# Optimization experiments

Hardware: AMD Instinct MI355X
Metric: run time of the kernel (lower is better)

## Reference

```python
import jax, jax.numpy as jnp
import numpy as np

N_NODES = 100000
N_EDGES = 1250000
NFEAT = 64
EDGE_DIM = 13
HID = 64
NREPEATS = 3
EPS = 1e-5


def setup_inputs() -> dict:
    key = jax.random.key(0)
    ks = jax.random.split(key, 16)
    s = lambda fan_in: 1.0 / np.sqrt(fan_in)
    return {
        "hx": jax.random.normal(ks[0], (N_NODES, NFEAT), dtype=jnp.float32),
        "edge_index": jax.random.randint(ks[1], (2, N_EDGES), 0, N_NODES, dtype=jnp.int64),
        "edgefeats": jax.random.normal(ks[2], (N_EDGES, EDGE_DIM), dtype=jnp.float32),
        # fnet MLP: 13 -> 64 -> 64 -> NFEAT (last layer with bias, llbias=True)
        "fW1": jax.random.uniform(ks[3], (64, EDGE_DIM), jnp.float32, -s(EDGE_DIM), s(EDGE_DIM)),
        "fb1": jax.random.uniform(ks[4], (64,), jnp.float32, -s(EDGE_DIM), s(EDGE_DIM)),
        "fW2": jax.random.uniform(ks[5], (64, 64), jnp.float32, -s(64), s(64)),
        "fb2": jax.random.uniform(ks[6], (64,), jnp.float32, -s(64), s(64)),
        "fW3": jax.random.uniform(ks[7], (NFEAT, 64), jnp.float32, -s(64), s(64)),
        "fb3": jax.random.uniform(ks[8], (NFEAT,), jnp.float32, -s(64), s(64)),
        # GRUCellEx params
        "Wih": jax.random.uniform(ks[9], (3 * HID, NFEAT), jnp.float32, -s(HID), s(HID)),
        "Whh": jax.random.uniform(ks[10], (3 * HID, HID), jnp.float32, -s(HID), s(HID)),
        "bih": jax.random.uniform(ks[11], (3 * HID,), jnp.float32, -s(HID), s(HID)),
        "bhh": jax.random.uniform(ks[12], (3 * HID,), jnp.float32, -s(HID), s(HID)),
        "Wig": jax.random.uniform(ks[13], (NFEAT, HID), jnp.float32, -s(HID), s(HID)),
        "big": jax.random.uniform(ks[14], (NFEAT,), jnp.float32, -s(HID), s(HID)),
    }


def _inorm(g):
    # InstanceNorm1d(1 channel): normalize each row over its 3H features, biased var
    mu = jnp.mean(g, axis=-1, keepdims=True)
    var = jnp.mean(jnp.square(g - mu), axis=-1, keepdims=True)
    return (g - mu) * jax.lax.rsqrt(var + EPS)


def reference(hx, edge_index, edgefeats, fW1, fb1, fW2, fb2, fW3, fb3,
              Wih, Whh, bih, bhh, Wig, big):
    # fnet: per-edge weight vector [E, NFEAT] (vv=True)
    w = jax.nn.relu(edgefeats @ fW1.T + fb1)
    w = jax.nn.relu(w @ fW2.T + fb2)
    w = w @ fW3.T + fb3

    # flow='target_to_source': gather from edge_index[1], aggregate at edge_index[0]
    dst = edge_index[0]
    src = edge_index[1]
    deg = jax.ops.segment_sum(jnp.ones((src.shape[0],), jnp.float32), dst,
                              num_segments=hx.shape[0])
    inv_deg = 1.0 / jnp.maximum(deg, 1.0)

    bih_r, bih_i, bih_n = jnp.split(bih, 3)
    bhh_r, bhh_i, bhh_n = jnp.split(bhh, 3)

    hxs = [hx]
    for _ in range(NREPEATS):
        # NNConv (vv): message = x_j * w, mean aggregation
        msg = hx[src] * w                                   # [E, F]
        agg = jax.ops.segment_sum(msg, dst, num_segments=hx.shape[0]) * inv_deg[:, None]
        # GRUCellEx: input gate on hidden
        inp = jax.nn.sigmoid(hx @ Wig.T + big) * agg
        gi = _inorm(inp @ Wih.T)                            # [N, 3H]
        gh = _inorm(hx @ Whh.T)
        i_r, i_i, i_n = jnp.split(gi, 3, axis=1)
        h_r, h_i, h_n = jnp.split(gh, 3, axis=1)
        resetgate = jax.nn.sigmoid(i_r + bih_r + h_r + bhh_r)
        inputgate = jax.nn.sigmoid(i_i + bih_i + h_i + bhh_i)
        newgate = jnp.tanh(i_n + bih_n + resetgate * (h_n + bhh_n))
        hx = newgate + inputgate * (hx - newgate)
        hxs.append(hx)
    return jnp.concatenate(hxs, axis=1)                     # [N, F*(NREPEATS+1)]
```

## Files before the change

### kernel.cpp

```cpp
#include <hip/hip_runtime.h>
#include <math.h>

#define NN 100000
#define NE 1250000
#define EPSI 1e-5f

#define WS_W        0ull
#define WS_AGG      160000000ull
#define WS_WB       185600000ull
#define WS_INVDEG   264000000ull
#define WS_COUNTS   264400000ull
#define WS_ROWSTART 264800000ull
#define WS_CURSOR   265200128ull
#define WS_BSUM     265600128ull
#define WS_BSUMEX   265601792ull
#define WS_SRC      265603584ull
#define WS_EPERM    270603584ull

#define WB_TOTAL 37888

typedef unsigned short u16;
typedef unsigned int u32;
typedef short s16x4 __attribute__((ext_vector_type(4)));
typedef short s16x8 __attribute__((ext_vector_type(8)));
typedef float f32x4 __attribute__((ext_vector_type(4)));
typedef u32 u32x4 __attribute__((ext_vector_type(4)));
typedef u32 u32x2 __attribute__((ext_vector_type(2)));
typedef float f32x4u __attribute__((ext_vector_type(4), aligned(4)));

__device__ __forceinline__ u16 f2bf(float f) {
    u32 u = __float_as_uint(f);
    return (u16)((u + 0x7fffu + ((u >> 16) & 1u)) >> 16);
}
__device__ __forceinline__ float bf2f(u16 b) {
    return __uint_as_float(((u32)b) << 16);
}
__device__ __forceinline__ u32 cvtpk(float lo, float hi) {
    u32 r;
    asm("v_cvt_pk_bf16_f32 %0, %1, %2" : "=v"(r) : "v"(lo), "v"(hi));
    return r;
}
__device__ __forceinline__ float sigmoidf_(float x) {
    return 1.f / (1.f + __expf(-x));
}
__device__ __forceinline__ float tanhf_(float x) {
    float e = __expf(2.f * x);
    return 1.f - 2.f / (e + 1.f);
}
__device__ __forceinline__ s16x8 lds_frag(const u16* p) {
    s16x4 lo = *(const s16x4*)p;
    s16x4 hi = *(const s16x4*)(p + 4);
    return __builtin_shufflevector(lo, hi, 0, 1, 2, 3, 4, 5, 6, 7);
}
__device__ __forceinline__ s16x8 gfrag(const u16* W, int n, int ks, int q) {
    return *(const s16x8*)(W + n * 64 + ks * 32 + q * 8);
}
__device__ __forceinline__ float unpk(const u32* p, int r) {
    u32 v = p[r >> 1];
    return bf2f((u16)((r & 1) ? (v >> 16) : (v & 0xffffu)));
}

__global__ __launch_bounds__(256) void k_fnet_mfma(
    const float* __restrict__ ef,
    const float* __restrict__ b1, const float* __restrict__ b2,
    const float* __restrict__ b3,
    const int* __restrict__ eperm,
    const u16* __restrict__ wbf,
    u16* __restrict__ wout)
{
    __shared__ u16 w1l[64 * 16];
    __shared__ u16 w2l[64 * 68];
    __shared__ u16 w3l[64 * 68];
    __shared__ u16 hbuf[4][32 * 68];

    int tid = threadIdx.x;
    const u16* wf1 = wbf + 28672;
    const u16* wf2 = wbf + 29696;
    const u16* wf3 = wbf + 33792;
    if (tid < 128)
        *(u32x4*)(&w1l[tid * 8]) = *(const u32x4*)(wf1 + tid * 8);
    for (int c = tid; c < 512; c += 256) {
        int n = c >> 3, cc = c & 7;
        u32x4 v2 = *(const u32x4*)(wf2 + c * 8);
        u32x4 v3 = *(const u32x4*)(wf3 + c * 8);
        u16* p2 = &w2l[n * 68 + cc * 8];
        u16* p3 = &w3l[n * 68 + cc * 8];
        *(u32x2*)p2       = __builtin_shufflevector(v2, v2, 0, 1);
        *(u32x2*)(p2 + 4) = __builtin_shufflevector(v2, v2, 2, 3);
        *(u32x2*)p3       = __builtin_shufflevector(v3, v3, 0, 1);
        *(u32x2*)(p3 + 4) = __builtin_shufflevector(v3, v3, 2, 3);
    }
    __syncthreads();

    int wave = tid >> 6, lane = tid & 63;
    int q = lane >> 4, t = lane & 15;
    int ebase = blockIdx.x * 128 + wave * 32;
    u16* hb = hbuf[wave];

    f32x4 b1v = *(const f32x4*)(b1 + 4 * t);
    f32x4 b2v = *(const f32x4*)(b2 + 4 * t);
    f32x4 b3v = *(const f32x4*)(b3 + 4 * t);

    const s16x8 zfrag = {0, 0, 0, 0, 0, 0, 0, 0};

    s16x8 a1[2];
#pragma unroll
    for (int mi = 0; mi < 2; ++mi) {
        int e = ebase + mi * 16 + t;
        u32 xp[4] = {0u, 0u, 0u, 0u};
        if (e < NE) {
            const float* ep = ef + (size_t)e * 13;
            if (q == 0) {
                f32x4u v0 = *(const f32x4u*)(ep);
                f32x4u v1 = *(const f32x4u*)(ep + 4);
                xp[0] = cvtpk(v0[0], v0[1]); xp[1] = cvtpk(v0[2], v0[3]);
                xp[2] = cvtpk(v1[0], v1[1]); xp[3] = cvtpk(v1[2], v1[3]);
            } else if (q == 1) {
                f32x4u v0 = *(const f32x4u*)(ep + 8);
                float v12 = ep[12];
                xp[0] = cvtpk(v0[0], v0[1]); xp[1] = cvtpk(v0[2], v0[3]);
                xp[2] = cvtpk(v12, 0.f);
            }
        }
        a1[mi] = __builtin_bit_cast(s16x8, *(u32x4*)xp);
    }

    s16x8 B1f[4];
#pragma unroll
    for (int ni = 0; ni < 4; ++ni) {
        s16x8 b = zfrag;
        if (q < 2) b = lds_frag(&w1l[(ni * 16 + t) * 16 + q * 8]);
        B1f[ni] = b;
    }

    f32x4 h1[4][2];
#pragma unroll
    for (int ni = 0; ni < 4; ++ni)
#pragma unroll
        for (int mi = 0; mi < 2; ++mi) {
            f32x4 acc = {b1v[ni], b1v[ni], b1v[ni], b1v[ni]};
            acc = __builtin_amdgcn_mfma_f32_16x16x32_bf16(a1[mi], B1f[ni], acc, 0, 0, 0);
            h1[ni][mi] = acc;
        }
#pragma unroll
    for (int mi = 0; mi < 2; ++mi)
#pragma unroll
        for (int r = 0; r < 4; ++r) {
            u32 lo = cvtpk(fmaxf(h1[0][mi][r], 0.f), fmaxf(h1[1][mi][r], 0.f));
            u32 hi = cvtpk(fmaxf(h1[2][mi][r], 0.f), fmaxf(h1[3][mi][r], 0.f));
            u32x2 v = {lo, hi};
            *(u32x2*)(&hb[(mi * 16 + q * 4 + r) * 68 + 4 * t]) = v;
        }

    s16x8 a2[2][2];
#pragma unroll
    for (int mi = 0; mi < 2; ++mi)
#pragma unroll
        for (int ks = 0; ks < 2; ++ks)
            a2[mi][ks] = lds_frag(&hb[(mi * 16 + t) * 68 + ks * 32 + q * 8]);
    f32x4 h2[4][2];
#pragma unroll
    for (int ni = 0; ni < 4; ++ni) {
        s16x8 w0 = lds_frag(&w2l[(ni * 16 + t) * 68 + q * 8]);
        s16x8 w1_ = lds_frag(&w2l[(ni * 16 + t) * 68 + 32 + q * 8]);
#pragma unroll
        for (int mi = 0; mi < 2; ++mi) {
            f32x4 acc = {b2v[ni], b2v[ni], b2v[ni], b2v[ni]};
            acc = __builtin_amdgcn_mfma_f32_16x16x32_bf16(a2[mi][0], w0, acc, 0, 0, 0);
            acc = __builtin_amdgcn_mfma_f32_16x16x32_bf16(a2[mi][1], w1_, acc, 0, 0, 0);
            h2[ni][mi] = acc;
        }
    }
#pragma unroll
    for (int mi = 0; mi < 2; ++mi)
#pragma unroll
        for (int r = 0; r < 4; ++r) {
            u32 lo = cvtpk(fmaxf(h2[0][mi][r], 0.f), fmaxf(h2[1][mi][r], 0.f));
            u32 hi = cvtpk(fmaxf(h2[2][mi][r], 0.f), fmaxf(h2[3][mi][r], 0.f));
            u32x2 v = {lo, hi};
            *(u32x2*)(&hb[(mi * 16 + q * 4 + r) * 68 + 4 * t]) = v;
        }

    s16x8 a3[2][2];
#pragma unroll
    for (int mi = 0; mi < 2; ++mi)
#pragma unroll
        for (int ks = 0; ks < 2; ++ks)
            a3[mi][ks] = lds_frag(&hb[(mi * 16 + t) * 68 + ks * 32 + q * 8]);
    f32x4 h3[4][2];
#pragma unroll
    for (int ni = 0; ni < 4; ++ni) {
        s16x8 w0 = lds_frag(&w3l[(ni * 16 + t) * 68 + q * 8]);
        s16x8 w1_ = lds_frag(&w3l[(ni * 16 + t) * 68 + 32 + q * 8]);
#pragma unroll
        for (int mi = 0; mi < 2; ++mi) {
            f32x4 acc = {b3v[ni], b3v[ni], b3v[ni], b3v[ni]};
            acc = __builtin_amdgcn_mfma_f32_16x16x32_bf16(a3[mi][0], w0, acc, 0, 0, 0);
            acc = __builtin_amdgcn_mfma_f32_16x16x32_bf16(a3[mi][1], w1_, acc, 0, 0, 0);
            h3[ni][mi] = acc;
        }
    }
    int base0 = ebase + q * 4;
    int base1 = ebase + 16 + q * 4;
    int4 pos0 = *(const int4*)(eperm + ((base0 + 3 < NE) ? base0 : 0));
    int4 pos1 = *(const int4*)(eperm + ((base1 + 3 < NE) ? base1 : 0));
#pragma unroll
    for (int mi = 0; mi < 2; ++mi)
#pragma unroll
        for (int r = 0; r < 4; ++r) {
            int e = ebase + mi * 16 + q * 4 + r;
            if (e < NE) {
                int pos = mi ? ((const int*)&pos1)[r] : ((const int*)&pos0)[r];
                u32x2 v = {cvtpk(h3[0][mi][r], h3[1][mi][r]),
                           cvtpk(h3[2][mi][r], h3[3][mi][r])};
                *(u32x2*)(wout + (size_t)pos * 64 + 4 * t) = v;
            }
        }
}

__global__ void k_prep_w(const float* __restrict__ Wig, const float* __restrict__ Whh,
                         const float* __restrict__ Wih,
                         const float* __restrict__ W1, const float* __restrict__ W2,
                         const float* __restrict__ W3, u16* __restrict__ wb)
{
    int i = blockIdx.x * 256 + threadIdx.x;
    if (i >= WB_TOTAL) return;
    float v;
    if (i < 4096) {
        int n = i >> 6, k = i & 63;
        int pn = ((n & 15) << 2) + (n >> 4);
        v = Wig[pn * 64 + k];
    } else if (i < 16384) {
        int j = i - 4096;
        int n = j >> 6, k = j & 63;
        int g = n >> 6, m = n & 63;
        int pm = ((m & 15) << 2) + (m >> 4);
        v = Whh[(g * 64 + pm) * 64 + k];
    } else if (i < 28672) {
        int j = i - 16384;
        int n = j >> 6, k = j & 63;
        int g = n >> 6, m = n & 63;
        int pm = ((m & 15) << 2) + (m >> 4);
        v = Wih[(g * 64 + pm) * 64 + k];
    } else if (i < 29696) {
        int j = i - 28672;
        int n = j >> 4, k = j & 15;
        int pn = ((n & 15) << 2) + (n >> 4);
        v = (k < 13) ? W1[pn * 13 + k] : 0.f;
    } else if (i < 33792) {
        int j = i - 29696;
        int n = j >> 6, k = j & 63;
        int pn = ((n & 15) << 2) + (n >> 4);
        v = W2[pn * 64 + k];
    } else {
        int j = i - 33792;
        int n = j >> 6, k = j & 63;
        int pn = ((n & 15) << 2) + (n >> 4);
        v = W3[pn * 64 + k];
    }
    wb[i] = f2bf(v);
}

__global__ void k_count(const int* __restrict__ idx, int* __restrict__ counts)
{
    int e = blockIdx.x * 256 + threadIdx.x;
    if (e < NE) atomicAdd(&counts[idx[e]], 1);
}

__global__ void k_scan_partial(const int* __restrict__ counts, int* __restrict__ bsum)
{
    __shared__ int s[256];
    int i = blockIdx.x * 256 + threadIdx.x;
    int v = (i < NN) ? counts[i] : 0;
    s[threadIdx.x] = v; __syncthreads();
    for (int off = 128; off > 0; off >>= 1) {
        if (threadIdx.x < off) s[threadIdx.x] += s[threadIdx.x + off];
        __syncthreads();
    }
    if (threadIdx.x == 0) bsum[blockIdx.x] = s[0];
}

__global__ void k_scan_bsum(const int* __restrict__ bsum, int* __restrict__ bsumex)
{
    __shared__ int s[512];
    int t = threadIdx.x;
    int v0 = (t < 391) ? bsum[t] : 0;
    s[t] = v0; __syncthreads();
    for (int off = 1; off < 512; off <<= 1) {
        int add = (t >= off) ? s[t - off] : 0;
        __syncthreads();
        s[t] += add;
        __syncthreads();
    }
    if (t < 391) bsumex[t] = s[t] - v0;
}

__global__ void k_scan_final(const int* __restrict__ counts, const int* __restrict__ bsumex,
                             int* __restrict__ rowstart, int* __restrict__ cursor,
                             float* __restrict__ invdeg)
{
    __shared__ int s[256];
    int t = threadIdx.x;
    int i = blockIdx.x * 256 + t;
    int c = (i < NN) ? counts[i] : 0;
    s[t] = c; __syncthreads();
    for (int off = 1; off < 256; off <<= 1) {
        int add = (t >= off) ? s[t - off] : 0;
        __syncthreads();
        s[t] += add;
        __syncthreads();
    }
    int ex = s[t] - c + bsumex[blockIdx.x];
    if (i < NN) {
        rowstart[i] = ex;
        cursor[i] = ex;
        invdeg[i] = 1.f / (float)(c > 1 ? c : 1);
    }
    if (i == 0) rowstart[NN] = NE;
}

__global__ void k_scatter(const int* __restrict__ idx, int* __restrict__ cursor,
                          int* __restrict__ srcs, int* __restrict__ eperm)
{
    int e = blockIdx.x * 256 + threadIdx.x;
    if (e < NE) {
        int d = idx[e];
        int s = idx[NE + e];
        int p = atomicAdd(&cursor[d], 1);
        __builtin_nontemporal_store(s, &srcs[p]);
        eperm[e] = p;
    }
}

__global__ void k_init(const float4* __restrict__ hx4, float* __restrict__ outp)
{
    int i = blockIdx.x * 256 + threadIdx.x;
    int n = i >> 4, q = i & 15;
    ((float4*)(outp + (size_t)n * 256))[q] = hx4[i];
}

__global__ __launch_bounds__(256) void k_agg(
    const float* __restrict__ outp, const u16* __restrict__ w,
    const int* __restrict__ srcs, const int* __restrict__ rowstart,
    const float* __restrict__ invdeg, float* __restrict__ agg, int it)
{
    int lane = threadIdx.x & 63;
    int g = lane >> 4, t = lane & 15;
    int n = blockIdx.x * 4 + (threadIdx.x >> 6);
    n = __builtin_amdgcn_readfirstlane(n);
    int p0 = rowstart[n], p1 = rowstart[n + 1];
    const float* hxb = outp + (size_t)it * 64 + 4 * t;
    f32x4 accA = {0.f, 0.f, 0.f, 0.f};
    f32x4 accB = {0.f, 0.f, 0.f, 0.f};
    int p = p0;
    for (; p + 8 <= p1; p += 8) {
        int sA = srcs[p + g];
        int sB = srcs[p + 4 + g];
        f32x4 hA = *(const f32x4*)(hxb + (size_t)sA * 256);
        f32x4 hB = *(const f32x4*)(hxb + (size_t)sB * 256);
        s16x4 wA = __builtin_nontemporal_load((const s16x4*)(w + (size_t)(p + g) * 64 + 4 * t));
        s16x4 wB = __builtin_nontemporal_load((const s16x4*)(w + (size_t)(p + 4 + g) * 64 + 4 * t));
#pragma unroll
        for (int j = 0; j < 4; ++j) {
            accA[j] = fmaf(hA[j], bf2f((u16)wA[j]), accA[j]);
            accB[j] = fmaf(hB[j], bf2f((u16)wB[j]), accB[j]);
        }
    }
    if (p + 4 <= p1) {
        int sA = srcs[p + g];
        f32x4 hA = *(const f32x4*)(hxb + (size_t)sA * 256);
        s16x4 wA = __builtin_nontemporal_load((const s16x4*)(w + (size_t)(p + g) * 64 + 4 * t));
#pragma unroll
        for (int j = 0; j < 4; ++j)
            accA[j] = fmaf(hA[j], bf2f((u16)wA[j]), accA[j]);
        p += 4;
    }
    int rem = p1 - p;
    if (g < rem) {
        int sB = srcs[p + g];
        f32x4 hB = *(const f32x4*)(hxb + (size_t)sB * 256);
        s16x4 wB = __builtin_nontemporal_load((const s16x4*)(w + (size_t)(p + g) * 64 + 4 * t));
#pragma unroll
        for (int j = 0; j < 4; ++j)
            accB[j] = fmaf(hB[j], bf2f((u16)wB[j]), accB[j]);
    }
#pragma unroll
    for (int j = 0; j < 4; ++j) accA[j] += accB[j];
#pragma unroll
    for (int j = 0; j < 4; ++j) {
        accA[j] += __shfl_xor(accA[j], 16, 64);
        accA[j] += __shfl_xor(accA[j], 32, 64);
    }
    if (g == 0) {
        float inv = invdeg[n];
        f32x4 o = {accA[0] * inv, accA[1] * inv, accA[2] * inv, accA[3] * inv};
        *(f32x4*)(agg + (size_t)n * 64 + 4 * t) = o;
    }
}

__global__ __launch_bounds__(256) void k_gru_fused(
    float* __restrict__ outp, const float* __restrict__ agg,
    const u16* __restrict__ wb,
    const float* __restrict__ big, const float* __restrict__ bih,
    const float* __restrict__ bhh, int it)
{
    __shared__ u16 hbuf[4][16 * 68];
    int tid = threadIdx.x;
    int wave = tid >> 6, lane = tid & 63;
    int q = lane >> 4, t = lane & 15;
    int nbase = blockIdx.x * 64 + wave * 16;
    u16* hb = hbuf[wave];
    const u16* wigb = wb;
    const u16* whhb = wb + 4096;
    const u16* wihb = wb + 16384;

    {
        int c = lane & 15;
        int mrow = lane >> 4;
#pragma unroll
        for (int rep = 0; rep < 4; ++rep) {
            int m = rep * 4 + mrow;
            int node = nbase + m;
            float4 v = make_float4(0.f, 0.f, 0.f, 0.f);
            if (node < NN)
                v = *(const float4*)(outp + (size_t)node * 256 + (size_t)it * 64 + c * 4);
            u32x2 pk = {cvtpk(v.x, v.y), cvtpk(v.z, v.w)};
            *(u32x2*)(&hb[m * 68 + c * 4]) = pk;
        }
    }

    s16x8 ahx[2];
    ahx[0] = lds_frag(&hb[t * 68 + q * 8]);
    ahx[1] = lds_frag(&hb[t * 68 + 32 + q * 8]);
    u32 hxpk[4][2];
#pragma unroll
    for (int r = 0; r < 4; ++r)
        *(u32x2*)hxpk[r] = *(const u32x2*)(&hb[(q * 4 + r) * 68 + 4 * t]);

    f32x4 bgv = *(const f32x4*)(big + 4 * t);
    f32x4 gacc[4];
#pragma unroll
    for (int ni = 0; ni < 4; ++ni) {
        s16x8 b0 = gfrag(wigb, ni * 16 + t, 0, q);
        s16x8 b1 = gfrag(wigb, ni * 16 + t, 1, q);
        f32x4 acc = {bgv[ni], bgv[ni], bgv[ni], bgv[ni]};
        acc = __builtin_amdgcn_mfma_f32_16x16x32_bf16(ahx[0], b0, acc, 0, 0, 0);
        acc = __builtin_amdgcn_mfma_f32_16x16x32_bf16(ahx[1], b1, acc, 0, 0, 0);
        gacc[ni] = acc;
    }
#pragma unroll
    for (int r = 0; r < 4; ++r) {
        int node = nbase + q * 4 + r;
        f32x4 av = {0.f, 0.f, 0.f, 0.f};
        if (node < NN) av = *(const f32x4*)(agg + (size_t)node * 64 + 4 * t);
        float i0 = sigmoidf_(gacc[0][r]) * av[0];
        float i1 = sigmoidf_(gacc[1][r]) * av[1];
        float i2 = sigmoidf_(gacc[2][r]) * av[2];
        float i3 = sigmoidf_(gacc[3][r]) * av[3];
        u32x2 pk = {cvtpk(i0, i1), cvtpk(i2, i3)};
        *(u32x2*)(&hb[(q * 4 + r) * 68 + 4 * t]) = pk;
    }

    float sgh[4] = {0.f, 0.f, 0.f, 0.f}, qgh[4] = {0.f, 0.f, 0.f, 0.f};
    u32 ghp[12][2];
#pragma unroll
    for (int ni = 0; ni < 12; ++ni) {
        s16x8 b0 = gfrag(whhb, ni * 16 + t, 0, q);
        s16x8 b1 = gfrag(whhb, ni * 16 + t, 1, q);
        f32x4 acc = {0.f, 0.f, 0.f, 0.f};
        acc = __builtin_amdgcn_mfma_f32_16x16x32_bf16(ahx[0], b0, acc, 0, 0, 0);
        acc = __builtin_amdgcn_mfma_f32_16x16x32_bf16(ahx[1], b1, acc, 0, 0, 0);
#pragma unroll
        for (int r = 0; r < 4; ++r) { sgh[r] += acc[r]; qgh[r] += acc[r] * acc[r]; }
        ghp[ni][0] = cvtpk(acc[0], acc[1]);
        ghp[ni][1] = cvtpk(acc[2], acc[3]);
    }

    s16x8 ain[2];
    ain[0] = lds_frag(&hb[t * 68 + q * 8]);
    ain[1] = lds_frag(&hb[t * 68 + 32 + q * 8]);

    float sgi[4] = {0.f, 0.f, 0.f, 0.f}, qgi[4] = {0.f, 0.f, 0.f, 0.f};
    u32 gip[12][2];
#pragma unroll
    for (int ni = 0; ni < 12; ++ni) {
        s16x8 b0 = gfrag(wihb, ni * 16 + t, 0, q);
        s16x8 b1 = gfrag(wihb, ni * 16 + t, 1, q);
        f32x4 acc = {0.f, 0.f, 0.f, 0.f};
        acc = __builtin_amdgcn_mfma_f32_16x16x32_bf16(ain[0], b0, acc, 0, 0, 0);
        acc = __builtin_amdgcn_mfma_f32_16x16x32_bf16(ain[1], b1, acc, 0, 0, 0);
#pragma unroll
        for (int r = 0; r < 4; ++r) { sgi[r] += acc[r]; qgi[r] += acc[r] * acc[r]; }
        gip[ni][0] = cvtpk(acc[0], acc[1]);
        gip[ni][1] = cvtpk(acc[2], acc[3]);
    }

#pragma unroll
    for (int m = 1; m < 16; m <<= 1) {
#pragma unroll
        for (int r = 0; r < 4; ++r) {
            sgh[r] += __shfl_xor(sgh[r], m, 64);
            qgh[r] += __shfl_xor(qgh[r], m, 64);
            sgi[r] += __shfl_xor(sgi[r], m, 64);
            qgi[r] += __shfl_xor(qgi[r], m, 64);
        }
    }
    float mi_[4], ri_[4], mh_[4], rh_[4];
#pragma unroll
    for (int r = 0; r < 4; ++r) {
        mi_[r] = sgi[r] * (1.f / 192.f);
        mh_[r] = sgh[r] * (1.f / 192.f);
        ri_[r] = rsqrtf(qgi[r] * (1.f / 192.f) - mi_[r] * mi_[r] + EPSI);
        rh_[r] = rsqrtf(qgh[r] * (1.f / 192.f) - mh_[r] * mh_[r] + EPSI);
    }

    f32x4 bihr = *(const f32x4*)(bih + 4 * t);
    f32x4 bihi = *(const f32x4*)(bih + 64 + 4 * t);
    f32x4 bihn = *(const f32x4*)(bih + 128 + 4 * t);
    f32x4 bhhr = *(const f32x4*)(bhh + 4 * t);
    f32x4 bhhi = *(const f32x4*)(bhh + 64 + 4 * t);
    f32x4 bhhn = *(const f32x4*)(bhh + 128 + 4 * t);
#pragma unroll
    for (int r = 0; r < 4; ++r) {
        int node = nbase + q * 4 + r;
        f32x4 res;
#pragma unroll
        for (int ni = 0; ni < 4; ++ni) {
            float iv_r = (unpk(gip[ni], r) - mi_[r]) * ri_[r];
            float iv_i = (unpk(gip[ni + 4], r) - mi_[r]) * ri_[r];
            float iv_n = (unpk(gip[ni + 8], r) - mi_[r]) * ri_[r];
            float hv_r = (unpk(ghp[ni], r) - mh_[r]) * rh_[r];
            float hv_i = (unpk(ghp[ni + 4], r) - mh_[r]) * rh_[r];
            float hv_n = (unpk(ghp[ni + 8], r) - mh_[r]) * rh_[r];
            float rg = sigmoidf_(iv_r + bihr[ni] + hv_r + bhhr[ni]);
            float zg = sigmoidf_(iv_i + bihi[ni] + hv_i + bhhi[ni]);
            float ng = tanhf_(iv_n + bihn[ni] + rg * (hv_n + bhhn[ni]));
            float ho = bf2f((u16)((ni & 1) ? (hxpk[r][ni >> 1] >> 16)
                                           : (hxpk[r][ni >> 1] & 0xffffu)));
            res[ni] = ng + zg * (ho - ng);
        }
        if (node < NN)
            *(f32x4*)(outp + (size_t)node * 256 + (size_t)(it + 1) * 64 + 4 * t) = res;
    }
}

extern "C" void kernel_launch(void* const* d_in, const int* in_sizes, int n_in,
                              void* d_out, int out_size, void* d_ws, size_t ws_size,
                              hipStream_t stream)
{
    const float* hx  = (const float*)d_in[0];
    const int*   eix = (const int*)d_in[1];
    const float* ef  = (const float*)d_in[2];
    const float* fW1 = (const float*)d_in[3];
    const float* fb1 = (const float*)d_in[4];
    const float* fW2 = (const float*)d_in[5];
    const float* fb2 = (const float*)d_in[6];
    const float* fW3 = (const float*)d_in[7];
    const float* fb3 = (const float*)d_in[8];
    const float* Wih = (const float*)d_in[9];
    const float* Whh = (const float*)d_in[10];
    const float* bih = (const float*)d_in[11];
    const float* bhh = (const float*)d_in[12];
    const float* Wig = (const float*)d_in[13];
    const float* big = (const float*)d_in[14];
    float* outp = (float*)d_out;
    char* ws = (char*)d_ws;

    u16*    w      = (u16*)(ws + WS_W);
    float*  agg    = (float*)(ws + WS_AGG);
    u16*    wb     = (u16*)(ws + WS_WB);
    float*  invdeg = (float*)(ws + WS_INVDEG);
    int*    counts = (int*)(ws + WS_COUNTS);
    int*    rowst  = (int*)(ws + WS_ROWSTART);
    int*    cursor = (int*)(ws + WS_CURSOR);
    int*    bsum   = (int*)(ws + WS_BSUM);
    int*    bsumex = (int*)(ws + WS_BSUMEX);
    int*    srcs   = (int*)(ws + WS_SRC);
    int*    eperm  = (int*)(ws + WS_EPERM);

    hipMemsetAsync(counts, 0, NN * sizeof(int), stream);
    k_prep_w<<<(WB_TOTAL + 255) / 256, 256, 0, stream>>>(Wig, Whh, Wih, fW1, fW2, fW3, wb);
    k_count<<<(NE + 255) / 256, 256, 0, stream>>>(eix, counts);
    k_scan_partial<<<391, 256, 0, stream>>>(counts, bsum);
    k_scan_bsum<<<1, 512, 0, stream>>>(bsum, bsumex);
    k_scan_final<<<391, 256, 0, stream>>>(counts, bsumex, rowst, cursor, invdeg);
    k_scatter<<<(NE + 255) / 256, 256, 0, stream>>>(eix, cursor, srcs, eperm);
    k_fnet_mfma<<<9766, 256, 0, stream>>>(ef, fb1, fb2, fb3, eperm, wb, w);
    k_init<<<6250, 256, 0, stream>>>((const float4*)hx, outp);

    for (int it = 0; it < 3; ++it) {
        k_agg<<<25000, 256, 0, stream>>>(outp, w, srcs, rowst, invdeg, agg, it);
        k_gru_fused<<<1563, 256, 0, stream>>>(outp, agg, wb, big, bih, bhh, it);
    }
}
```

Baseline: 805.7 us.

## Replace atomic cursor scatter with 8-way privatized rank counting for CSR build

The CSR construction now records each edge's rank from the counting atomic into one of 8 sub-histograms, selected by block index. A new kernel turns those sub-counts into per-slot offsets, and the final pass computes positions without a second atomic pass. This removes one full round of contended atomics on the cursor array and spreads contention across 8 copies. The cost is a larger memset and an extra small kernel, and the temporary counts reuse the agg buffer.

```diff
diff --git a/kernel.cpp b/kernel.cpp
--- a/kernel.cpp
+++ b/kernel.cpp
@@ -261,10 +261,28 @@
     wb[i] = f2bf(v);
 }
 
-__global__ void k_count(const int* __restrict__ idx, int* __restrict__ counts)
+__global__ void k_rank(const int* __restrict__ idx, int* __restrict__ cnt8,
+                       int* __restrict__ rank_out)
 {
     int e = blockIdx.x * 256 + threadIdx.x;
-    if (e < NE) atomicAdd(&counts[idx[e]], 1);
+    int k = blockIdx.x & 7;
+    if (e < NE) {
+        int d = idx[e];
+        int r = atomicAdd(&cnt8[k * NN + d], 1);
+        rank_out[e] = r;
+    }
+}
+
+__global__ void k_sumcnt(int* __restrict__ cnt8, int* __restrict__ counts)
+{
+    int d = blockIdx.x * 256 + threadIdx.x;
+    if (d >= NN) return;
+    int c[8], run = 0;
+#pragma unroll
+    for (int k = 0; k < 8; ++k) c[k] = cnt8[k * NN + d];
+#pragma unroll
+    for (int k = 0; k < 8; ++k) { int t = c[k]; cnt8[k * NN + d] = run; run += t; }
+    counts[d] = run;
 }
 
 __global__ void k_scan_partial(const int* __restrict__ counts, int* __restrict__ bsum)
@@ -296,8 +314,7 @@
 }
 
 __global__ void k_scan_final(const int* __restrict__ counts, const int* __restrict__ bsumex,
-                             int* __restrict__ rowstart, int* __restrict__ cursor,
-                             float* __restrict__ invdeg)
+                             int* __restrict__ rowstart, float* __restrict__ invdeg)
 {
     __shared__ int s[256];
     int t = threadIdx.x;
@@ -313,22 +330,24 @@
     int ex = s[t] - c + bsumex[blockIdx.x];
     if (i < NN) {
         rowstart[i] = ex;
-        cursor[i] = ex;
         invdeg[i] = 1.f / (float)(c > 1 ? c : 1);
     }
     if (i == 0) rowstart[NN] = NE;
 }
 
-__global__ void k_scatter(const int* __restrict__ idx, int* __restrict__ cursor,
-                          int* __restrict__ srcs, int* __restrict__ eperm)
+__global__ void k_finalize(const int* __restrict__ idx, const int* __restrict__ cnt8,
+                           const int* __restrict__ rowstart,
+                           int* __restrict__ eperm, int* __restrict__ srcs)
 {
     int e = blockIdx.x * 256 + threadIdx.x;
     if (e < NE) {
         int d = idx[e];
         int s = idx[NE + e];
-        int p = atomicAdd(&cursor[d], 1);
+        int k = (e >> 8) & 7;
+        int r = eperm[e];
+        int p = rowstart[d] + cnt8[k * NN + d] + r;
+        eperm[e] = p;
         __builtin_nontemporal_store(s, &srcs[p]);
-        eperm[e] = p;
     }
 }
 
@@ -568,23 +587,24 @@
 
     u16*    w      = (u16*)(ws + WS_W);
     float*  agg    = (float*)(ws + WS_AGG);
+    int*    cnt8   = (int*)(ws + WS_AGG);
     u16*    wb     = (u16*)(ws + WS_WB);
     float*  invdeg = (float*)(ws + WS_INVDEG);
     int*    counts = (int*)(ws + WS_COUNTS);
     int*    rowst  = (int*)(ws + WS_ROWSTART);
-    int*    cursor = (int*)(ws + WS_CURSOR);
     int*    bsum   = (int*)(ws + WS_BSUM);
     int*    bsumex = (int*)(ws + WS_BSUMEX);
     int*    srcs   = (int*)(ws + WS_SRC);
     int*    eperm  = (int*)(ws + WS_EPERM);
 
-    hipMemsetAsync(counts, 0, NN * sizeof(int), stream);
+    hipMemsetAsync(cnt8, 0, 8 * NN * sizeof(int), stream);
     k_prep_w<<<(WB_TOTAL + 255) / 256, 256, 0, stream>>>(Wig, Whh, Wih, fW1, fW2, fW3, wb);
-    k_count<<<(NE + 255) / 256, 256, 0, stream>>>(eix, counts);
+    k_rank<<<(NE + 255) / 256, 256, 0, stream>>>(eix, cnt8, eperm);
+    k_sumcnt<<<391, 256, 0, stream>>>(cnt8, counts);
     k_scan_partial<<<391, 256, 0, stream>>>(counts, bsum);
     k_scan_bsum<<<1, 512, 0, stream>>>(bsum, bsumex);
-    k_scan_final<<<391, 256, 0, stream>>>(counts, bsumex, rowst, cursor, invdeg);
-    k_scatter<<<(NE + 255) / 256, 256, 0, stream>>>(eix, cursor, srcs, eperm);
+    k_scan_final<<<391, 256, 0, stream>>>(counts, bsumex, rowst, invdeg);
+    k_finalize<<<(NE + 255) / 256, 256, 0, stream>>>(eix, cnt8, rowst, eperm, srcs);
     k_fnet_mfma<<<9766, 256, 0, stream>>>(ef, fb1, fb2, fb3, eperm, wb, w);
     k_init<<<6250, 256, 0, stream>>>((const float4*)hx, outp);
 
```

Result: faster. 752.6 us (-6.6%).
